# Kernel optimization log

Measured on AMD Instinct MI355X. Metric: run time of the kernel, lower is better.

Reference implementation:

```python
import jax, jax.numpy as jnp
import numpy as np

DIM = 2048
H = 16           # n_heads
KV = 4           # n_kv_heads
G = H // KV      # gqa factor
CQ = 128         # q_compressed_dim
QN, QR = 96, 32  # q nope / rope head dims
CKV = 128        # kv_compressed_dim
KN, KR = 64, 64  # k nope / rope head dims
VD = 256         # v_head_dim
THETA = 10000.0


def _t5_layer_norm(x, gamma, eps=1e-5):
    mu = jnp.mean(x, axis=-1, keepdims=True)
    var = jnp.var(x, axis=-1, keepdims=True)
    return (x - mu) * jax.lax.rsqrt(var + eps) * gamma


def _rope(x):
    # x: [B, H, S, D] with interleaved even/odd rotation, positions = arange(S)
    S, D = x.shape[-2], x.shape[-1]
    inv_freq = 1.0 / THETA ** (jnp.arange(0, D, 2, dtype=jnp.float32) / D)
    ang = jnp.arange(S, dtype=jnp.float32)[:, None] * inv_freq  # [S, D/2]
    cos = jnp.cos(ang).astype(x.dtype)
    sin = jnp.sin(ang).astype(x.dtype)
    xe, xo = x[..., ::2], x[..., 1::2]
    re = xe * cos - xo * sin
    ro = xe * sin + xo * cos
    return jnp.stack((re, ro), axis=-1).reshape(x.shape)


def setup_inputs() -> dict:
    key = jax.random.key(0)
    ks = jax.random.split(key, 7)
    s = 0.02
    return {
        "x": jax.random.normal(ks[0], (2, 2048, DIM), dtype=jnp.float32),
        "w_dq": jax.random.normal(ks[1], (DIM, CQ), dtype=jnp.float32) * s,
        "gamma_q": jnp.ones((CQ,), dtype=jnp.float32),
        "w_uq": jax.random.normal(ks[2], (CQ, H * (QN + QR)), dtype=jnp.float32) * s,
        "w_dkv": jax.random.normal(ks[3], (DIM, CKV + KR), dtype=jnp.float32) * s,
        "gamma_kv": jnp.ones((CKV,), dtype=jnp.float32),
        "w_ukv": jax.random.normal(ks[4], (CKV, KV * (KN + VD)), dtype=jnp.float32) * s,
        "w_o": jax.random.normal(ks[5], (H * VD, DIM), dtype=jnp.float32) * s,
    }


def reference(x, w_dq, gamma_q, w_uq, w_dkv, gamma_kv, w_ukv, w_o):
    B, S, _ = x.shape
    # low-rank Q path
    cq = _t5_layer_norm(x @ w_dq, gamma_q)                     # [B,S,CQ]
    q = cq @ w_uq                                              # [B,S,H*(QN+QR)]
    q_nope = q[..., : H * QN].reshape(B, S, H, QN).transpose(0, 2, 1, 3)
    q_rope = q[..., H * QN :].reshape(B, S, H, QR).transpose(0, 2, 1, 3)
    q_rope = _rope(q_rope)
    q_states = jnp.concatenate((q_nope, q_rope), axis=-1)      # [B,H,S,QN+QR]

    # low-rank KV path + decoupled shared rope key
    ckv_kr = x @ w_dkv                                         # [B,S,CKV+KR]
    ckv = _t5_layer_norm(ckv_kr[..., :CKV], gamma_kv)
    k_rope = _rope(ckv_kr[..., CKV:][:, None, :, :])           # [B,1,S,KR]
    kv = ckv @ w_ukv                                           # [B,S,KV*(KN+VD)]
    k_nope = kv[..., : KV * KN].reshape(B, S, KV, KN).transpose(0, 2, 1, 3)
    v_states = kv[..., KV * KN :].reshape(B, S, KV, VD).transpose(0, 2, 1, 3)
    k_states = jnp.concatenate(
        (k_nope, jnp.broadcast_to(k_rope, (B, KV, S, KR))), axis=-1
    )                                                          # [B,KV,S,KN+KR]

    # grouped-query attention: broadcast kv heads instead of materializing repeats
    dqk = QN + QR  # == KN + KR == 128
    qg = q_states.reshape(B, KV, G, S, dqk)
    scores = jnp.einsum("bgrqd,bgkd->bgrqk", qg, k_states) / jnp.sqrt(
        jnp.asarray(dqk, dtype=x.dtype)
    )
    causal = jnp.triu(jnp.ones((S, S), dtype=bool), k=1)
    scores = jnp.where(causal, -jnp.inf, scores)
    attn = jax.nn.softmax(scores, axis=-1)
    out = jnp.einsum("bgrqk,bgkv->bgrqv", attn, v_states)      # [B,KV,G,S,VD]
    out = out.reshape(B, H, S, VD).transpose(0, 2, 1, 3).reshape(B, S, H * VD)
    return out @ w_o
```

## Files before the change

kernel.cpp:

```cpp
#include <hip/hip_runtime.h>
#include <hip/hip_bf16.h>
#include <math.h>

#define DIM   2048
#define S_LEN 2048
#define BATCH 2
#define NH    16
#define NKV   4
#define CQ_   128
#define QN_   96
#define QR_   32
#define CKV_  128
#define KN_   64
#define KR_   64
#define VD_   256
#define ROWS_TOT (BATCH*S_LEN)
#define QK_SCALE 0.08838834764831845f
#define LOG2E    1.4426950408889634f

typedef __attribute__((ext_vector_type(8)))  short short8;
typedef __attribute__((ext_vector_type(4)))  short short4v;
typedef __attribute__((ext_vector_type(4)))  float float4v;
typedef __attribute__((ext_vector_type(16))) float float16v;
typedef __attribute__((ext_vector_type(4)))  int   int4v;

__device__ inline short f2bf(float x) {
    union { __hip_bfloat16 h; short s; } u;
    u.h = __float2bfloat16(x);
    return u.s;
}

__device__ __forceinline__ void gl_lds16(const short* g, short* lds) {
    __builtin_amdgcn_global_load_lds(
        (const __attribute__((address_space(1))) unsigned int*)(g),
        (__attribute__((address_space(3))) unsigned int*)(lds),
        16, 0, 0);
}


__global__ __launch_bounds__(256)
void kprep_all(const float* __restrict__ x, const float* __restrict__ w_o,
               const float* __restrict__ w_uq, const float* __restrict__ w_ukv,
               const float* __restrict__ w_dq, const float* __restrict__ w_dkv,
               short* __restrict__ xbf, short* __restrict__ w_oT,
               short* __restrict__ w_uqT, short* __restrict__ w_ukvT,
               short* __restrict__ wdT, float* __restrict__ tq,
               float* __restrict__ tk)
{
    const int bid = blockIdx.x, tid = threadIdx.x;
    if (bid < 4096) {
        int i = bid * 2048 + tid * 8;
        float4 a = *reinterpret_cast<const float4*>(x + i);
        float4 b = *reinterpret_cast<const float4*>(x + i + 4);
        short8 o;
        o[0] = f2bf(a.x); o[1] = f2bf(a.y); o[2] = f2bf(a.z); o[3] = f2bf(a.w);
        o[4] = f2bf(b.x); o[5] = f2bf(b.y); o[6] = f2bf(b.z); o[7] = f2bf(b.w);
        *reinterpret_cast<short8*>(xbf + i) = o;
        return;
    }
    if (bid >= 6408) {
        int gid = (bid - 6408) * 256 + tid;
        int spos = gid / 48, e = gid - spos * 48;
        if (e < 16) {
            float inv = powf(10000.f, -(float)(2 * e) / 32.f);
            float sn, c; sincosf((float)spos * inv, &sn, &c);
            tq[(spos * 16 + e) * 2 + 0] = c;
            tq[(spos * 16 + e) * 2 + 1] = sn;
        } else {
            int i2 = e - 16;
            float inv = powf(10000.f, -(float)(2 * i2) / 64.f);
            float sn, c; sincosf((float)spos * inv, &sn, &c);
            tk[(spos * 32 + i2) * 2 + 0] = c;
            tk[(spos * 32 + i2) * 2 + 1] = sn;
        }
        return;
    }

    __shared__ float tf[64][65];
    const int tb = bid - 4096;
    int lb, nct, R; short* dst;
    if (tb < 2048)      { lb = tb;        nct = 32; R = 4096; dst = w_oT;   }
    else if (tb < 2112) { lb = tb - 2048; nct = 32; R = 128;  dst = w_uqT;  }
    else if (tb < 2152) { lb = tb - 2112; nct = 20; R = 128;  dst = w_ukvT; }
    else                { lb = tb - 2152; nct = 5;  R = 2048; dst = wdT;    }
    const int ct = lb % nct, rt = lb / nct;
    const int r0 = rt * 64, c0 = ct * 64;
    const float* src; int stride, nbase;
    if (tb < 2048)      { src = w_o;   stride = 2048; nbase = c0; }
    else if (tb < 2112) { src = w_uq;  stride = 2048; nbase = c0; }
    else if (tb < 2152) { src = w_ukv; stride = 1280; nbase = c0; }
    else if (ct < 2)    { src = w_dq;  stride = 128;  nbase = c0; }
    else                { src = w_dkv; stride = 192;  nbase = c0 - 128; }

    #pragma unroll
    for (int u4 = 0; u4 < 4; ++u4) {
        int u = u4 * 256 + tid;
        int kr = u >> 4, nc = (u & 15) * 4;
        float4 v = *reinterpret_cast<const float4*>(&src[(size_t)(r0 + kr) * stride + nbase + nc]);
        tf[kr][nc + 0] = v.x; tf[kr][nc + 1] = v.y;
        tf[kr][nc + 2] = v.z; tf[kr][nc + 3] = v.w;
    }
    __syncthreads();
    #pragma unroll
    for (int u2 = 0; u2 < 2; ++u2) {
        int u = u2 * 256 + tid;
        int nr = u >> 3, kc8 = (u & 7) * 8;
        short8 o;
        #pragma unroll
        for (int j = 0; j < 8; ++j) o[j] = f2bf(tf[kc8 + j][nr]);
        *reinterpret_cast<short8*>(&dst[(size_t)(c0 + nr) * R + r0 + kc8]) = o;
    }
}

__global__ __launch_bounds__(256)
void k1_mfma(const short* __restrict__ xbf, const short* __restrict__ wdT,
             const float* __restrict__ gamma_q, const float* __restrict__ gamma_kv,
             const float* __restrict__ tk,
             short* __restrict__ cq_bf, short* __restrict__ ckv_bf,
             float* __restrict__ kr_rope)
{
    __shared__ float ys[16][321];
    __shared__ float st[16][4];
    const int tid = threadIdx.x, lane = tid & 63, w = tid >> 6;
    const int g = lane >> 4, l15 = lane & 15;
    const int m0 = blockIdx.x * 16;
    const int wn0 = w * 80;

    float4v acc[5];
    #pragma unroll
    for (int nj = 0; nj < 5; ++nj) acc[nj] = (float4v){0.f, 0.f, 0.f, 0.f};

    const short* arow = xbf + (size_t)(m0 + l15) * 2048 + g * 8;
    for (int ks = 0; ks < 64; ++ks) {
        short8 a = *reinterpret_cast<const short8*>(arow + ks * 32);
        #pragma unroll
        for (int nj = 0; nj < 5; ++nj) {
            short8 bf = *reinterpret_cast<const short8*>(
                wdT + (size_t)(wn0 + nj * 16 + l15) * 2048 + ks * 32 + g * 8);
            acc[nj] = __builtin_amdgcn_mfma_f32_16x16x32_bf16(a, bf, acc[nj], 0, 0, 0);
        }
    }

    #pragma unroll
    for (int nj = 0; nj < 5; ++nj)
        #pragma unroll
        for (int r = 0; r < 4; ++r)
            ys[g * 4 + r][wn0 + nj * 16 + l15] = acc[nj][r];
    __syncthreads();

    if (tid < 32) {
        int row = tid >> 1, seg = tid & 1, base = seg * 128;
        float s1 = 0.f, s2 = 0.f;
        for (int j = 0; j < 128; ++j) { float v = ys[row][base + j]; s1 += v; s2 += v * v; }
        float mu  = s1 * (1.f / 128.f);
        float var = s2 * (1.f / 128.f) - mu * mu;
        st[row][seg * 2 + 0] = mu;
        st[row][seg * 2 + 1] = rsqrtf(var + 1e-5f);
    }
    __syncthreads();

    for (int i = tid; i < 16 * 320; i += 256) {
        int row = i / 320, col = i - row * 320;
        int r = m0 + row, spos = r & (S_LEN - 1);
        float v = ys[row][col];
        if (col < 128) {
            cq_bf[(size_t)r * CQ_ + col] =
                f2bf((v - st[row][0]) * st[row][1] * gamma_q[col] * (QK_SCALE * LOG2E));
        } else if (col < 256) {
            ckv_bf[(size_t)r * CKV_ + (col - 128)] =
                f2bf((v - st[row][2]) * st[row][3] * gamma_kv[col - 128]);
        } else {
            int d = col - 256, i2 = d >> 1;
            float xe = ys[row][256 + (d & ~1)];
            float xo = ys[row][256 + (d | 1)];
            float c  = tk[(spos * 32 + i2) * 2 + 0];
            float sn = tk[(spos * 32 + i2) * 2 + 1];
            kr_rope[(size_t)r * KR_ + d] = (d & 1) ? (xe * sn + xo * c)
                                                   : (xe * c - xo * sn);
        }
    }
}

__global__ __launch_bounds__(256)
void k23_fused(const short* __restrict__ cq_bf, const short* __restrict__ w_uqT,
               const float* __restrict__ tq, short* __restrict__ q_states,
               const short* __restrict__ ckv_bf, const short* __restrict__ w_ukvT,
               const float* __restrict__ kr_rope,
               short* __restrict__ k_frag, short* __restrict__ v_frag)
{
    const int tid = threadIdx.x, lane = tid & 63, w = tid >> 6;
    const int g = lane >> 4, l15 = lane & 15;

    if (blockIdx.x < 512) {
        const int bm = blockIdx.x >> 1, ns = blockIdx.x & 1;
        const int m0 = bm * 16;
        const int nb = ns * 1024 + w * 256;

        short8 af[4];
        #pragma unroll
        for (int ks = 0; ks < 4; ++ks)
            af[ks] = *reinterpret_cast<const short8*>(
                cq_bf + (size_t)(m0 + l15) * 128 + ks * 32 + g * 8);

        float4v acc[16];
        #pragma unroll
        for (int nj = 0; nj < 16; ++nj) acc[nj] = (float4v){0.f, 0.f, 0.f, 0.f};

        #pragma unroll
        for (int ks = 0; ks < 4; ++ks)
            #pragma unroll
            for (int nj = 0; nj < 16; ++nj) {
                short8 bf = *reinterpret_cast<const short8*>(
                    w_uqT + (size_t)(nb + nj * 16 + l15) * 128 + ks * 32 + g * 8);
                acc[nj] = __builtin_amdgcn_mfma_f32_16x16x32_bf16(af[ks], bf, acc[nj], 0, 0, 0);
            }

        #pragma unroll
        for (int nj = 0; nj < 16; ++nj) {
            int j = nb + nj * 16 + l15;
            if (j < NH * QN_) {
                int h = j / QN_, d = j - h * QN_;
                #pragma unroll
                for (int r = 0; r < 4; ++r) {
                    int rg = m0 + g * 4 + r, bb = rg >> 11, spos = rg & (S_LEN - 1);
                    q_states[(((size_t)bb * NH + h) * S_LEN + spos) * 128 + d] =
                        f2bf(acc[nj][r]);
                }
            } else {
                int jj = j - NH * QN_;
                int h = jj >> 5, d = jj & 31, i2 = d >> 1;
                #pragma unroll
                for (int r = 0; r < 4; ++r) {
                    int rg = m0 + g * 4 + r, bb = rg >> 11, spos = rg & (S_LEN - 1);
                    float v = acc[nj][r];
                    float p = __shfl_xor(v, 1, 64);
                    float c  = tq[(spos * 16 + i2) * 2 + 0];
                    float sn = tq[(spos * 16 + i2) * 2 + 1];
                    float out = (d & 1) ? (p * sn + v * c) : (v * c - p * sn);
                    q_states[(((size_t)bb * NH + h) * S_LEN + spos) * 128 + QN_ + d] =
                        f2bf(out);
                }
            }
        }
    } else {
        const int m0 = (blockIdx.x - 512) * 16;
        const int nb = w * 320;

        short8 af[4];
        #pragma unroll
        for (int ks = 0; ks < 4; ++ks)
            af[ks] = *reinterpret_cast<const short8*>(
                ckv_bf + (size_t)(m0 + l15) * 128 + ks * 32 + g * 8);

        float4v acc[20];
        #pragma unroll
        for (int nj = 0; nj < 20; ++nj) acc[nj] = (float4v){0.f, 0.f, 0.f, 0.f};

        #pragma unroll
        for (int ks = 0; ks < 4; ++ks)
            #pragma unroll
            for (int nj = 0; nj < 20; ++nj) {
                short8 bf = *reinterpret_cast<const short8*>(
                    w_ukvT + (size_t)(nb + nj * 16 + l15) * 128 + ks * 32 + g * 8);
                acc[nj] = __builtin_amdgcn_mfma_f32_16x16x32_bf16(af[ks], bf, acc[nj], 0, 0, 0);
            }

        #pragma unroll
        for (int nj = 0; nj < 20; ++nj) {
            int j = nb + nj * 16 + l15;
            if (j < NKV * KN_) {
                int kvh = j >> 6, d = j & 63;
                int stf = d >> 4, hif = (d >> 3) & 1, jo = d & 7;
                #pragma unroll
                for (int r = 0; r < 4; ++r) {
                    int rg = m0 + g * 4 + r, bb = rg >> 11, spos = rg & (S_LEN - 1);
                    int bk = bb * NKV + kvh;
                    size_t idx = ((size_t)(bk * 32 + (spos >> 6)) * 1024
                                  + ((spos >> 5) & 1) * 512 + stf * 64 + hif * 32
                                  + (spos & 31)) * 8 + jo;
                    k_frag[idx] = f2bf(acc[nj][r]);
                }
            } else {
                int jj = j - NKV * KN_;
                int kvh = jj >> 8, d = jj & 255;
                int dt5 = d >> 5, l31d = d & 31;
                #pragma unroll
                for (int r = 0; r < 4; ++r) {
                    int rg = m0 + g * 4 + r, bb = rg >> 11, spos = rg & (S_LEN - 1);
                    int bk = bb * NKV + kvh;
                    size_t slot = (size_t)(bk * 32 + (spos >> 6)) * 2048
                                  + dt5 * 256 + ((spos & 63) >> 5) * 128
                                  + ((spos >> 4) & 1) * 64 + ((spos >> 3) & 1) * 32 + l31d;
                    v_frag[slot * 8 + (spos & 7)] = f2bf(acc[nj][r]);
                }
            }
        }

        for (int i = tid; i < 16 * KR_; i += 256) {
            int rr = i >> 6, dd = i & 63;
            int rg = m0 + rr, bb = rg >> 11, spos = rg & (S_LEN - 1);
            short vv = f2bf(kr_rope[(size_t)rg * KR_ + dd]);
            int d = 64 + dd;
            int stf = d >> 4, hif = (d >> 3) & 1, jo = d & 7;
            size_t ubase = ((size_t)(spos >> 6)) * 1024
                           + ((spos >> 5) & 1) * 512 + stf * 64 + hif * 32 + (spos & 31);
            #pragma unroll
            for (int kvh = 0; kvh < NKV; ++kvh) {
                int bk = bb * NKV + kvh;
                k_frag[((size_t)bk * 32 * 1024 + ubase) * 8 + jo] = vv;
            }
        }
    }
}

__global__ __launch_bounds__(512, 1)
void k4_attn_mfma(const short* __restrict__ q_states,
                  const short* __restrict__ k_frag,
                  const short* __restrict__ v_frag,
                  short* __restrict__ attn_out)
{
    __shared__ __align__(16) short ks_lds[3][8192];
    __shared__ __align__(16) short vt_lds[2][16384];

    const int tid = threadIdx.x, lane = tid & 63, w = tid >> 6;
    const int l31 = lane & 31, hi = lane >> 5;
    const int g = w & 3, h = w >> 2;
    const int bid = blockIdx.x;
    const int qt = (bid < 256) ? (15 - (bid >> 5)) : (7 - ((bid - 256) >> 5));
    const int bh = bid & 31;
    const int h_head = bh & 15, b = bh >> 4, kvh = h_head >> 2;
    const int bk = b * NKV + kvh;

    const short* kfbase = k_frag + (size_t)bk * 32 * 8192;
    const short* vfbase = v_frag + (size_t)bk * 32 * 16384;

    const int qrow0 = qt * 128 + g * 32;
    const int qglob = qrow0 + l31;

    short8 qcur[8];
    {
        const short* qr = q_states +
            (((size_t)b * NH + h_head) * S_LEN + qrow0 + l31) * 128 + hi * 8;
        #pragma unroll
        for (int st = 0; st < 8; ++st)
            qcur[st] = *reinterpret_cast<const short8*>(qr + st * 16);
    }

    float16v o[8];
    #pragma unroll
    for (int dt = 0; dt < 8; ++dt)
        #pragma unroll
        for (int r = 0; r < 16; ++r) o[dt][r] = 0.f;
    float mreg = -1e30f, lreg = 0.f;

    const int nkt = 2 * (qt + 1);

    auto issueK = [&](int kt, int bufi) {
        const short* src = kfbase + (size_t)kt * 8192;
        #pragma unroll
        for (int i = 0; i < 2; ++i) {
            int c = w * 2 + i;
            gl_lds16(src + c * 512 + lane * 8, &ks_lds[bufi][c * 512]);
        }
    };
    auto issueV = [&](int kt, int bufi) {
        const short* src = vfbase + (size_t)kt * 16384;
        #pragma unroll
        for (int i = 0; i < 4; ++i) {
            int c = w * 4 + i;
            gl_lds16(src + c * 512 + lane * 8, &vt_lds[bufi][c * 512]);
        }
    };

    issueK(0, 0);
    issueV(0, 0);
    issueK(1, 1);

    for (int seq = 0; seq < nkt; ++seq) {
        if (seq < nkt - 1) { asm volatile("s_waitcnt vmcnt(2)" ::: "memory"); }
        else               { asm volatile("s_waitcnt vmcnt(0)" ::: "memory"); }
        __builtin_amdgcn_s_barrier();
        __builtin_amdgcn_sched_barrier(0);

        if (seq + 1 < nkt) issueV(seq + 1, (seq + 1) & 1);
        if (seq + 2 < nkt) issueK(seq + 2, (seq + 2) % 3);

        const int kvb = seq * 64 + h * 32;
        if (kvb <= qrow0 + 31) {
            const short* kbuf = &ks_lds[seq % 3][h * 4096];
            float16v sa, sb;
            #pragma unroll
            for (int r = 0; r < 16; ++r) { sa[r] = 0.f; sb[r] = 0.f; }
            __builtin_amdgcn_s_setprio(1);
            #pragma unroll
            for (int st = 0; st < 8; st += 2) {
                short8 kf0 = *reinterpret_cast<const short8*>(kbuf + st * 512 + lane * 8);
                sa = __builtin_amdgcn_mfma_f32_32x32x16_bf16(kf0, qcur[st], sa, 0, 0, 0);
                short8 kf1 = *reinterpret_cast<const short8*>(kbuf + (st + 1) * 512 + lane * 8);
                sb = __builtin_amdgcn_mfma_f32_32x32x16_bf16(kf1, qcur[st + 1], sb, 0, 0, 0);
            }
            __builtin_amdgcn_s_setprio(0);
            float16v s;
            #pragma unroll
            for (int r = 0; r < 16; ++r) s[r] = sa[r] + sb[r];

            if (kvb + 31 > qglob || kvb + 31 > qrow0 + 31) {
                if (kvb + 31 > qrow0) {
                    #pragma unroll
                    for (int r = 0; r < 16; ++r) {
                        int kc = kvb + ((r & 3) + 8 * (r >> 2) + 4 * hi);
                        if (kc > qglob) s[r] = -1e30f;
                    }
                }
            }

            float mx = s[0];
            #pragma unroll
            for (int r = 1; r < 16; ++r) mx = fmaxf(mx, s[r]);
            mx = fmaxf(mx, __shfl_xor(mx, 32, 64));
            bool need = mx > mreg + 8.f;
            if (__ballot(need)) {
                float mnew = fmaxf(mreg, mx);
                float corr = exp2f(mreg - mnew);
                mreg = mnew;
                lreg *= corr;
                #pragma unroll
                for (int dt = 0; dt < 8; ++dt)
                    #pragma unroll
                    for (int r = 0; r < 16; ++r) o[dt][r] *= corr;
            }
            #pragma unroll
            for (int r = 0; r < 16; ++r) s[r] = exp2f(s[r] - mreg);
            float ps = 0.f;
            #pragma unroll
            for (int r = 0; r < 16; ++r) ps += s[r];
            ps += __shfl_xor(ps, 32, 64);
            lreg += ps;

            const short* vbuf = &vt_lds[seq & 1][h * 1024];
            __builtin_amdgcn_s_setprio(1);
            #pragma unroll
            for (int ks = 0; ks < 2; ++ks) {
                const int rb = ks * 8;
                int c01, c23, c45, c67;
                asm("v_cvt_pk_bf16_f32 %0, %1, %2" : "=v"(c01) : "v"(s[rb+0]), "v"(s[rb+1]));
                asm("v_cvt_pk_bf16_f32 %0, %1, %2" : "=v"(c23) : "v"(s[rb+2]), "v"(s[rb+3]));
                asm("v_cvt_pk_bf16_f32 %0, %1, %2" : "=v"(c45) : "v"(s[rb+4]), "v"(s[rb+5]));
                asm("v_cvt_pk_bf16_f32 %0, %1, %2" : "=v"(c67) : "v"(s[rb+6]), "v"(s[rb+7]));
                asm("v_permlane32_swap_b32 %0, %1" : "+v"(c01), "+v"(c45));
                asm("v_permlane32_swap_b32 %0, %1" : "+v"(c23), "+v"(c67));
                union { int4v i4; short8 s8; } u_;
                u_.i4.x = c01; u_.i4.y = c23; u_.i4.z = c45; u_.i4.w = c67;
                short8 pa = u_.s8;
                #pragma unroll
                for (int dt = 0; dt < 8; ++dt) {
                    short8 vf = *reinterpret_cast<const short8*>(
                        vbuf + dt * 2048 + ks * 512 + lane * 8);
                    o[dt] = __builtin_amdgcn_mfma_f32_32x32x16_bf16(vf, pa, o[dt], 0, 0, 0);
                }
            }
            __builtin_amdgcn_s_setprio(0);
        }
    }

    __syncthreads();
    {
        float* mlb = (float*)(&ks_lds[0][0]);
        mlb[w * 64 + lane] = mreg;
        mlb[512 + w * 64 + lane] = lreg;
    }
    __syncthreads();
    float s0f = 0.f, s1f = 0.f;
    if (h == 0) {
        float* mlb = (float*)(&ks_lds[0][0]);
        float m1 = mlb[(w + 4) * 64 + lane];
        float l1 = mlb[512 + (w + 4) * 64 + lane];
        float ms = fmaxf(mreg, m1);
        float c0 = exp2f(mreg - ms), c1 = exp2f(m1 - ms);
        float ls = lreg * c0 + l1 * c1;
        s0f = c0 / ls; s1f = c1 / ls;
    }
    float* cb = (float*)(&ks_lds[0][0]) + 1024;
    short* obase = attn_out + (((size_t)b * S_LEN + qglob) * NH + h_head) * VD_;
    for (int dt = 0; dt < 8; ++dt) {
        __syncthreads();
        if (h == 1) {
            #pragma unroll
            for (int r = 0; r < 16; ++r)
                cb[r * 256 + g * 64 + lane] = o[dt][r];
        }
        __syncthreads();
        if (h == 0) {
            #pragma unroll
            for (int r = 0; r < 16; ++r)
                o[dt][r] = o[dt][r] * s0f + cb[r * 256 + g * 64 + lane] * s1f;
            #pragma unroll
            for (int k4i = 0; k4i < 4; ++k4i) {
                int d0 = dt * 32 + k4i * 8 + hi * 4;
                short4v pk;
                #pragma unroll
                for (int j = 0; j < 4; ++j) pk[j] = f2bf(o[dt][k4i * 4 + j]);
                *reinterpret_cast<short4v*>(obase + d0) = pk;
            }
        }
    }
}

__global__ __launch_bounds__(256)
void k5_gemm_mfma(const short* __restrict__ A,
                  const short* __restrict__ Bt,
                  float* __restrict__ C)
{
    __shared__ __align__(16) short at[128 * 64];
    __shared__ __align__(16) short bt[128 * 64];
    const int tid  = threadIdx.x;
    const int lane = tid & 63;
    const int wid  = tid >> 6;
    const int wm = wid >> 1, wn = wid & 1;
    const int g = lane >> 4, l15 = lane & 15;
    const int swz = (blockIdx.x & 7) * 64 + (blockIdx.x >> 3);
    const int bm = swz & 31, bn = swz >> 5;
    const int m0 = bm * 128, n0 = bn * 128;

    float4v acc[4][4];
    #pragma unroll
    for (int mi = 0; mi < 4; ++mi)
        #pragma unroll
        for (int nj = 0; nj < 4; ++nj) acc[mi][nj] = (float4v){0.f, 0.f, 0.f, 0.f};

    for (int k0 = 0; k0 < 4096; k0 += 64) {
        __syncthreads();
        #pragma unroll
        for (int i = 0; i < 4; ++i) {
            int row = wid * 32 + i * 8 + (lane >> 3);
            int ch  = lane & 7;
            gl_lds16(A + (size_t)(m0 + row) * 4096 + k0 + ((ch ^ (row & 7)) * 8),
                     at + wid * 2048 + i * 512);
            gl_lds16(Bt + (size_t)(n0 + row) * 4096 + k0 + ((ch ^ (row & 7)) * 8),
                     bt + wid * 2048 + i * 512);
        }
        __syncthreads();

        #pragma unroll
        for (int kb = 0; kb < 2; ++kb) {
            short8 af[4], bfr[4];
            #pragma unroll
            for (int mi = 0; mi < 4; ++mi) {
                int row = wm * 64 + mi * 16 + l15;
                af[mi] = *reinterpret_cast<const short8*>(
                    at + row * 64 + (((g + 4 * kb) ^ (row & 7)) * 8));
            }
            #pragma unroll
            for (int nj = 0; nj < 4; ++nj) {
                int row = wn * 64 + nj * 16 + l15;
                bfr[nj] = *reinterpret_cast<const short8*>(
                    bt + row * 64 + (((g + 4 * kb) ^ (row & 7)) * 8));
            }
            #pragma unroll
            for (int mi = 0; mi < 4; ++mi)
                #pragma unroll
                for (int nj = 0; nj < 4; ++nj)
                    acc[mi][nj] = __builtin_amdgcn_mfma_f32_16x16x32_bf16(
                        af[mi], bfr[nj], acc[mi][nj], 0, 0, 0);
        }
    }

    #pragma unroll
    for (int mi = 0; mi < 4; ++mi)
        #pragma unroll
        for (int nj = 0; nj < 4; ++nj)
            #pragma unroll
            for (int r = 0; r < 4; ++r)
                C[(size_t)(m0 + wm * 64 + mi * 16 + g * 4 + r) * DIM + n0 + wn * 64 + nj * 16 + l15] =
                    acc[mi][nj][r];
}

extern "C" void kernel_launch(void* const* d_in, const int* in_sizes, int n_in,
                              void* d_out, int out_size, void* d_ws, size_t ws_size,
                              hipStream_t stream)
{
    const float* x        = (const float*)d_in[0];
    const float* w_dq     = (const float*)d_in[1];
    const float* gamma_q  = (const float*)d_in[2];
    const float* w_uq     = (const float*)d_in[3];
    const float* w_dkv    = (const float*)d_in[4];
    const float* gamma_kv = (const float*)d_in[5];
    const float* w_ukv    = (const float*)d_in[6];
    const float* w_o      = (const float*)d_in[7];
    float* out = (float*)d_out;

    char* ws = (char*)d_ws;
    float* kr_rope  = (float*)(ws);
    short* cq_bf    = (short*)(ws + (1ull  << 20));
    short* ckv_bf   = (short*)(ws + (2ull  << 20));
    float* tq       = (float*)(ws + (3ull  << 20));
    float* tk       = (float*)(ws + (4ull  << 20));
    short* w_uqT    = (short*)(ws + (5ull  << 20));
    short* w_ukvT   = (short*)(ws + (6ull  << 20));
    short* wdT      = (short*)(ws + (7ull  << 20));
    short* q_states = (short*)(ws + (9ull  << 20));
    short* k_frag   = (short*)(ws + (25ull << 20));
    short* v_frag   = (short*)(ws + (29ull << 20));
    short* attn_out = (short*)(ws + (37ull << 20));
    short* w_oT     = (short*)(ws + (69ull << 20));
    short* xbf      = (short*)(ws + (85ull << 20));

    kprep_all<<<dim3(6792), dim3(256), 0, stream>>>(
        x, w_o, w_uq, w_ukv, w_dq, w_dkv,
        xbf, w_oT, w_uqT, w_ukvT, wdT, tq, tk);

    k1_mfma<<<dim3(ROWS_TOT / 16), dim3(256), 0, stream>>>(
        xbf, wdT, gamma_q, gamma_kv, tk, cq_bf, ckv_bf, kr_rope);

    k23_fused<<<dim3(768), dim3(256), 0, stream>>>(
        cq_bf, w_uqT, tq, q_states, ckv_bf, w_ukvT, kr_rope, k_frag, v_frag);

    k4_attn_mfma<<<dim3(512), dim3(512), 0, stream>>>(
        q_states, k_frag, v_frag, attn_out);

    k5_gemm_mfma<<<dim3(512), dim3(256), 0, stream>>>(
        attn_out, w_oT, out);
}
```

Measured before the change: 269.0 us.

## Drop intra-block KV split in attention; use 256-thread blocks with two per CU

The attention kernel previously split each KV tile between two wave groups and merged their softmax states through LDS at the end. Now each 4-wave block walks all KV tiles in 32-key steps, and twice as many blocks are launched, with two resident per CU. K/V fragment layouts in the producer kernel are changed to 32-row tiles to match. This removes the cross-group merge and its barriers and is meant to improve scheduling, but it doubles the serial KV loop length per wave. It also pairs heavy and light causal query tiles in adjacent blocks.

```diff
diff --git a/kernel.cpp b/kernel.cpp
--- a/kernel.cpp
+++ b/kernel.cpp
@@ -275,9 +275,8 @@
                 for (int r = 0; r < 4; ++r) {
                     int rg = m0 + g * 4 + r, bb = rg >> 11, spos = rg & (S_LEN - 1);
                     int bk = bb * NKV + kvh;
-                    size_t idx = ((size_t)(bk * 32 + (spos >> 6)) * 1024
-                                  + ((spos >> 5) & 1) * 512 + stf * 64 + hif * 32
-                                  + (spos & 31)) * 8 + jo;
+                    size_t idx = ((size_t)(bk * 64 + (spos >> 5)) * 512
+                                  + stf * 64 + hif * 32 + (spos & 31)) * 8 + jo;
                     k_frag[idx] = f2bf(acc[nj][r]);
                 }
             } else {
@@ -288,9 +287,9 @@
                 for (int r = 0; r < 4; ++r) {
                     int rg = m0 + g * 4 + r, bb = rg >> 11, spos = rg & (S_LEN - 1);
                     int bk = bb * NKV + kvh;
-                    size_t slot = (size_t)(bk * 32 + (spos >> 6)) * 2048
-                                  + dt5 * 256 + ((spos & 63) >> 5) * 128
-                                  + ((spos >> 4) & 1) * 64 + ((spos >> 3) & 1) * 32 + l31d;
+                    size_t slot = (size_t)(bk * 64 + (spos >> 5)) * 1024
+                                  + dt5 * 128 + ((spos >> 4) & 1) * 64
+                                  + ((spos >> 3) & 1) * 32 + l31d;
                     v_frag[slot * 8 + (spos & 7)] = f2bf(acc[nj][r]);
                 }
             }
@@ -302,39 +301,37 @@
             short vv = f2bf(kr_rope[(size_t)rg * KR_ + dd]);
             int d = 64 + dd;
             int stf = d >> 4, hif = (d >> 3) & 1, jo = d & 7;
-            size_t ubase = ((size_t)(spos >> 6)) * 1024
-                           + ((spos >> 5) & 1) * 512 + stf * 64 + hif * 32 + (spos & 31);
+            size_t ubase = (size_t)(spos >> 5) * 512 + stf * 64 + hif * 32 + (spos & 31);
             #pragma unroll
             for (int kvh = 0; kvh < NKV; ++kvh) {
                 int bk = bb * NKV + kvh;
-                k_frag[((size_t)bk * 32 * 1024 + ubase) * 8 + jo] = vv;
-            }
-        }
-    }
-}
-
-__global__ __launch_bounds__(512, 1)
+                k_frag[((size_t)bk * 64 * 512 + ubase) * 8 + jo] = vv;
+            }
+        }
+    }
+}
+
+__global__ __launch_bounds__(256, 2)
 void k4_attn_mfma(const short* __restrict__ q_states,
                   const short* __restrict__ k_frag,
                   const short* __restrict__ v_frag,
                   short* __restrict__ attn_out)
 {
-    __shared__ __align__(16) short ks_lds[3][8192];
-    __shared__ __align__(16) short vt_lds[2][16384];
+    __shared__ __align__(16) short ks_lds[3][4096];
+    __shared__ __align__(16) short vt_lds[2][8192];
 
     const int tid = threadIdx.x, lane = tid & 63, w = tid >> 6;
     const int l31 = lane & 31, hi = lane >> 5;
-    const int g = w & 3, h = w >> 2;
-    const int bid = blockIdx.x;
-    const int qt = (bid < 256) ? (15 - (bid >> 5)) : (7 - ((bid - 256) >> 5));
-    const int bh = bid & 31;
+    const int u = blockIdx.x >> 1;
+    const int qt = (blockIdx.x & 1) ? (u >> 5) : (15 - (u >> 5));
+    const int bh = u & 31;
     const int h_head = bh & 15, b = bh >> 4, kvh = h_head >> 2;
     const int bk = b * NKV + kvh;
 
-    const short* kfbase = k_frag + (size_t)bk * 32 * 8192;
-    const short* vfbase = v_frag + (size_t)bk * 32 * 16384;
-
-    const int qrow0 = qt * 128 + g * 32;
+    const short* kfbase = k_frag + (size_t)bk * 64 * 4096;
+    const short* vfbase = v_frag + (size_t)bk * 64 * 8192;
+
+    const int qrow0 = qt * 128 + w * 32;
     const int qglob = qrow0 + l31;
 
     short8 qcur[8];
@@ -353,10 +350,10 @@
         for (int r = 0; r < 16; ++r) o[dt][r] = 0.f;
     float mreg = -1e30f, lreg = 0.f;
 
-    const int nkt = 2 * (qt + 1);
+    const int nkt = 4 * (qt + 1);
 
     auto issueK = [&](int kt, int bufi) {
-        const short* src = kfbase + (size_t)kt * 8192;
+        const short* src = kfbase + (size_t)kt * 4096;
         #pragma unroll
         for (int i = 0; i < 2; ++i) {
             int c = w * 2 + i;
@@ -364,7 +361,7 @@
         }
     };
     auto issueV = [&](int kt, int bufi) {
-        const short* src = vfbase + (size_t)kt * 16384;
+        const short* src = vfbase + (size_t)kt * 8192;
         #pragma unroll
         for (int i = 0; i < 4; ++i) {
             int c = w * 4 + i;
@@ -385,9 +382,9 @@
         if (seq + 1 < nkt) issueV(seq + 1, (seq + 1) & 1);
         if (seq + 2 < nkt) issueK(seq + 2, (seq + 2) % 3);
 
-        const int kvb = seq * 64 + h * 32;
+        const int kvb = seq * 32;
         if (kvb <= qrow0 + 31) {
-            const short* kbuf = &ks_lds[seq % 3][h * 4096];
+            const short* kbuf = ks_lds[seq % 3];
             float16v sa, sb;
             #pragma unroll
             for (int r = 0; r < 16; ++r) { sa[r] = 0.f; sb[r] = 0.f; }
@@ -404,19 +401,21 @@
             #pragma unroll
             for (int r = 0; r < 16; ++r) s[r] = sa[r] + sb[r];
 
-            if (kvb + 31 > qglob || kvb + 31 > qrow0 + 31) {
-                if (kvb + 31 > qrow0) {
-                    #pragma unroll
-                    for (int r = 0; r < 16; ++r) {
-                        int kc = kvb + ((r & 3) + 8 * (r >> 2) + 4 * hi);
-                        if (kc > qglob) s[r] = -1e30f;
-                    }
+            if (kvb + 31 > qrow0) {
+                #pragma unroll
+                for (int r = 0; r < 16; ++r) {
+                    int kc = kvb + ((r & 3) + 8 * (r >> 2) + 4 * hi);
+                    if (kc > qglob) s[r] = -1e30f;
                 }
             }
 
-            float mx = s[0];
-            #pragma unroll
-            for (int r = 1; r < 16; ++r) mx = fmaxf(mx, s[r]);
+            float mx = fmaxf(fmaxf(s[0], s[1]), s[2]);
+            float mx2 = fmaxf(fmaxf(s[3], s[4]), s[5]);
+            float mx3 = fmaxf(fmaxf(s[6], s[7]), s[8]);
+            float mx4 = fmaxf(fmaxf(s[9], s[10]), s[11]);
+            float mx5 = fmaxf(fmaxf(s[12], s[13]), s[14]);
+            mx = fmaxf(fmaxf(mx, mx2), mx3);
+            mx = fmaxf(fmaxf(mx, mx4), fmaxf(mx5, s[15]));
             mx = fmaxf(mx, __shfl_xor(mx, 32, 64));
             bool need = mx > mreg + 8.f;
             if (__ballot(need)) {
@@ -437,7 +436,7 @@
             ps += __shfl_xor(ps, 32, 64);
             lreg += ps;
 
-            const short* vbuf = &vt_lds[seq & 1][h * 1024];
+            const short* vbuf = vt_lds[seq & 1];
             __builtin_amdgcn_s_setprio(1);
             #pragma unroll
             for (int ks = 0; ks < 2; ++ks) {
@@ -455,7 +454,7 @@
                 #pragma unroll
                 for (int dt = 0; dt < 8; ++dt) {
                     short8 vf = *reinterpret_cast<const short8*>(
-                        vbuf + dt * 2048 + ks * 512 + lane * 8);
+                        vbuf + dt * 1024 + ks * 512 + lane * 8);
                     o[dt] = __builtin_amdgcn_mfma_f32_32x32x16_bf16(vf, pa, o[dt], 0, 0, 0);
                 }
             }
@@ -463,46 +462,19 @@
         }
     }
 
-    __syncthreads();
     {
-        float* mlb = (float*)(&ks_lds[0][0]);
-        mlb[w * 64 + lane] = mreg;
-        mlb[512 + w * 64 + lane] = lreg;
-    }
-    __syncthreads();
-    float s0f = 0.f, s1f = 0.f;
-    if (h == 0) {
-        float* mlb = (float*)(&ks_lds[0][0]);
-        float m1 = mlb[(w + 4) * 64 + lane];
-        float l1 = mlb[512 + (w + 4) * 64 + lane];
-        float ms = fmaxf(mreg, m1);
-        float c0 = exp2f(mreg - ms), c1 = exp2f(m1 - ms);
-        float ls = lreg * c0 + l1 * c1;
-        s0f = c0 / ls; s1f = c1 / ls;
-    }
-    float* cb = (float*)(&ks_lds[0][0]) + 1024;
-    short* obase = attn_out + (((size_t)b * S_LEN + qglob) * NH + h_head) * VD_;
-    for (int dt = 0; dt < 8; ++dt) {
-        __syncthreads();
-        if (h == 1) {
-            #pragma unroll
-            for (int r = 0; r < 16; ++r)
-                cb[r * 256 + g * 64 + lane] = o[dt][r];
-        }
-        __syncthreads();
-        if (h == 0) {
-            #pragma unroll
-            for (int r = 0; r < 16; ++r)
-                o[dt][r] = o[dt][r] * s0f + cb[r * 256 + g * 64 + lane] * s1f;
+        float invl = 1.f / lreg;
+        short* obase = attn_out + (((size_t)b * S_LEN + qglob) * NH + h_head) * VD_;
+        #pragma unroll
+        for (int dt = 0; dt < 8; ++dt)
             #pragma unroll
             for (int k4i = 0; k4i < 4; ++k4i) {
                 int d0 = dt * 32 + k4i * 8 + hi * 4;
                 short4v pk;
                 #pragma unroll
-                for (int j = 0; j < 4; ++j) pk[j] = f2bf(o[dt][k4i * 4 + j]);
+                for (int j = 0; j < 4; ++j) pk[j] = f2bf(o[dt][k4i * 4 + j] * invl);
                 *reinterpret_cast<short4v*>(obase + d0) = pk;
             }
-        }
     }
 }
 
@@ -615,7 +587,7 @@
     k23_fused<<<dim3(768), dim3(256), 0, stream>>>(
         cq_bf, w_uqT, tq, q_states, ckv_bf, w_ukvT, kr_rope, k_frag, v_frag);
 
-    k4_attn_mfma<<<dim3(512), dim3(512), 0, stream>>>(
+    k4_attn_mfma<<<dim3(1024), dim3(256), 0, stream>>>(
         q_states, k_frag, v_frag, attn_out);
 
     k5_gemm_mfma<<<dim3(512), dim3(256), 0, stream>>>(
```

Measured after the change: 364.2 us. +35.4%, slower.
